# Performance work log

Measured on AMD Instinct MI355X. Metric: run time of the kernel, lower is better.

The kernel has to match this reference:

```python
import jax, jax.numpy as jnp
import numpy as np

B, N, DIM = 4, 2048, 1024
H, DH = 16, 64


def setup_inputs() -> dict:
    key = jax.random.key(0)
    k1, k2, k3 = jax.random.split(key, 3)
    x = jax.random.normal(k1, (B, N, DIM), dtype=jnp.float32)
    # nn.Linear weight layout: [out_features, in_features]; y = x @ W.T
    w_qkv = jax.random.normal(k2, (3 * H * DH, DIM), dtype=jnp.float32) * (DIM ** -0.5)
    w_out = jax.random.normal(k3, (DIM, H * DH), dtype=jnp.float32) * ((H * DH) ** -0.5)
    b_out = jnp.zeros((DIM,), dtype=jnp.float32)
    return {"x": x, "w_qkv": w_qkv, "w_out": w_out, "b_out": b_out}


def reference(x, w_qkv, w_out, b_out):
    scale = DH ** -0.5
    qkv = jnp.einsum('bnd,ed->bne', x, w_qkv)            # [B,N,3*H*DH]
    q, k, v = jnp.split(qkv, 3, axis=-1)
    def to_heads(t):
        return t.reshape(B, N, H, DH).transpose(0, 2, 1, 3)  # b h n d
    q, k, v = to_heads(q), to_heads(k), to_heads(v)
    scores = jnp.einsum('bhnd,bhmd->bhnm', q, k) * scale  # [B,H,N,N]
    att = jax.nn.softmax(scores, axis=-1)
    out = jnp.einsum('bhnm,bhmd->bhnd', att, v)
    out = out.transpose(0, 2, 1, 3).reshape(B, N, H * DH)  # b n (h d)
    return jnp.einsum('bne,de->bnd', out, w_out) + b_out
```

## Files before the change

### kernel.cpp

```cpp
#include <hip/hip_runtime.h>
#include <hip/hip_bf16.h>
#include <math.h>

#define B_   4
#define N_   2048
#define DIM_ 1024
#define H_   16
#define DH_  64
#define E3_  3072

typedef __attribute__((ext_vector_type(8))) short  s8v;
typedef __attribute__((ext_vector_type(4))) float  f4v;

__device__ __forceinline__ unsigned short f2bf_fast(float f) {
    return (unsigned short)((__builtin_bit_cast(unsigned int, f) + 0x8000u) >> 16);
}
__device__ __forceinline__ unsigned int pkbf(float a, float b) {
    unsigned int ua = __builtin_bit_cast(unsigned int, a) + 0x8000u;
    unsigned int ub = __builtin_bit_cast(unsigned int, b) + 0x8000u;
    return __builtin_amdgcn_perm(ub, ua, 0x07060302);
}

__device__ __forceinline__ void gload_lds16(const void* g, void* l) {
    __builtin_amdgcn_global_load_lds(
        (const __attribute__((address_space(1))) unsigned int*)(uintptr_t)g,
        (__attribute__((address_space(3))) unsigned int*)(uintptr_t)l,
        16, 0, 0);
}

__global__ __launch_bounds__(256) void cvt_bf16(
    const float* __restrict__ in, unsigned short* __restrict__ out, int n)
{
    const int i = (blockIdx.x * 256 + threadIdx.x) * 4;
    if (i < n) {
        float4 v = *(const float4*)(in + i);
        uint2 pk;
        pk.x = pkbf(v.x, v.y);
        pk.y = pkbf(v.z, v.w);
        *(uint2*)(out + i) = pk;
    }
}

template<int MODE>
__global__ __launch_bounds__(256) void gemm_mfma(
    const unsigned short* __restrict__ A,
    const unsigned short* __restrict__ Bw,
    const float* __restrict__ bias,
    unsigned short* __restrict__ Cb,
    unsigned short* __restrict__ Vt,
    float* __restrict__ Cf,
    int M, int Nc, int K)
{
    __shared__ unsigned short As[128 * 32];
    __shared__ unsigned short Bs[128 * 32];

    const int tid  = threadIdx.x;
    const int w    = tid >> 6;
    const int lane = tid & 63;
    const int quad = lane >> 4;
    const int l15  = lane & 15;
    const int wm   = w & 1, wn = w >> 1;
    const int m0   = blockIdx.y * 128, n0 = blockIdx.x * 128;

    const int srow = lane >> 2;
    const int sch  = (lane & 3) * 8;

    f4v acc[4][4];
    #pragma unroll
    for (int i = 0; i < 4; i++)
        #pragma unroll
        for (int j = 0; j < 4; j++) acc[i][j] = (f4v){0.f, 0.f, 0.f, 0.f};

    for (int k0 = 0; k0 < K; k0 += 32) {
        __syncthreads();
        #pragma unroll
        for (int i = 0; i < 2; i++) {
            const int rbase = w * 32 + i * 16;
            gload_lds16(A  + (size_t)(m0 + rbase + srow) * K + k0 + sch,
                        &As[rbase * 32]);
            gload_lds16(Bw + (size_t)(n0 + rbase + srow) * K + k0 + sch,
                        &Bs[rbase * 32]);
        }
        __syncthreads();

        s8v af[4], bf[4];
        #pragma unroll
        for (int i = 0; i < 4; i++) {
            af[i] = *(const s8v*)&As[(wm * 64 + i * 16 + l15) * 32 + quad * 8];
            bf[i] = *(const s8v*)&Bs[(wn * 64 + i * 16 + l15) * 32 + quad * 8];
        }
        #pragma unroll
        for (int ms = 0; ms < 4; ms++)
            #pragma unroll
            for (int ns = 0; ns < 4; ns++)
                acc[ms][ns] = __builtin_amdgcn_mfma_f32_16x16x32_bf16(
                    af[ms], bf[ns], acc[ms][ns], 0, 0, 0);
    }

    if (MODE == 0) {
        #pragma unroll
        for (int ns = 0; ns < 4; ns++) {
            const int colb = n0 + wn * 64 + ns * 16;
            if (colb < 2048) {
                const float mul = (colb < 1024) ? 0.18033688011112042f : 1.0f;
                #pragma unroll
                for (int ms = 0; ms < 4; ms++)
                    #pragma unroll
                    for (int r = 0; r < 4; r++) {
                        const int row = m0 + wm * 64 + ms * 16 + quad * 4 + r;
                        Cb[(size_t)row * Nc + colb + l15] = f2bf_fast(acc[ms][ns][r] * mul);
                    }
            } else {
                const int e = colb + l15 - 2048;
                const int h = e >> 6, d = e & 63;
                #pragma unroll
                for (int ms = 0; ms < 4; ms++) {
                    const int row = m0 + wm * 64 + ms * 16 + quad * 4;
                    const int b = row >> 11, n = row & 2047;
                    uint2 pk;
                    pk.x = pkbf(acc[ms][ns][0], acc[ms][ns][1]);
                    pk.y = pkbf(acc[ms][ns][2], acc[ms][ns][3]);
                    *(uint2*)&Vt[(((size_t)b * 16 + h) * 64 + d) * 2048 + n] = pk;
                }
            }
        }
    } else {
        #pragma unroll
        for (int ns = 0; ns < 4; ns++) {
            const float bz = bias[n0 + wn * 64 + ns * 16 + l15];
            #pragma unroll
            for (int ms = 0; ms < 4; ms++)
                #pragma unroll
                for (int r = 0; r < 4; r++) {
                    const int row = m0 + wm * 64 + ms * 16 + quad * 4 + r;
                    Cf[(size_t)row * Nc + n0 + wn * 64 + ns * 16 + l15] =
                        acc[ms][ns][r] + bz;
                }
        }
    }
}

__global__ __launch_bounds__(256, 2) void attn_mfma(
    const unsigned short* __restrict__ qkv,
    const unsigned short* __restrict__ vT,
    unsigned short* __restrict__ ao)
{
    __shared__ __align__(16) unsigned short Ks[2][64][72];
    __shared__ __align__(16) unsigned short Vs[2][64][72];
    __shared__ __align__(16) unsigned short Ps[256][72];

    const int tid  = threadIdx.x;
    const int w    = tid >> 6;
    const int lane = tid & 63;
    const int quad = lane >> 4;
    const int l15  = lane & 15;

    const int bh = blockIdx.y;
    const int b  = bh >> 4;
    const int h  = bh & 15;
    const int q0 = blockIdx.x * 256;

    const unsigned short* qp  = qkv + (size_t)b * N_ * E3_ + (size_t)h * DH_;
    const unsigned short* kp  = qp + 1024;
    const unsigned short* vtp = vT + (size_t)bh * 64 * 2048;

    const int srow0 = tid >> 3;
    const int srow1 = (tid + 256) >> 3;
    const int sc8   = (tid & 7) * 8;

    s8v bq[4][2];
    #pragma unroll
    for (int mt = 0; mt < 4; mt++) {
        const unsigned short* qrow =
            qp + (size_t)(q0 + w * 64 + mt * 16 + l15) * E3_;
        bq[mt][0] = *(const s8v*)(qrow + quad * 8);
        bq[mt][1] = *(const s8v*)(qrow + 32 + quad * 8);
    }

    s8v ones;
    #pragma unroll
    for (int i = 0; i < 8; i++) ones[i] = (short)0x3F80;

    f4v o_acc[4][4];
    #pragma unroll
    for (int mt = 0; mt < 4; mt++)
        #pragma unroll
        for (int nt = 0; nt < 4; nt++) o_acc[mt][nt] = (f4v){0.f, 0.f, 0.f, 0.f};
    f4v lacc[4];
    #pragma unroll
    for (int mt = 0; mt < 4; mt++) lacc[mt] = (f4v){0.f, 0.f, 0.f, 0.f};

    {
        s8v k0a = *(const s8v*)(kp + (size_t)srow0 * E3_ + sc8);
        s8v k1a = *(const s8v*)(kp + (size_t)srow1 * E3_ + sc8);
        s8v v0a = *(const s8v*)(vtp + (size_t)srow0 * 2048 + sc8);
        s8v v1a = *(const s8v*)(vtp + (size_t)srow1 * 2048 + sc8);
        *(s8v*)&Ks[0][srow0][sc8] = k0a;
        *(s8v*)&Ks[0][srow1][sc8] = k1a;
        *(s8v*)&Vs[0][srow0][sc8] = v0a;
        *(s8v*)&Vs[0][srow1][sc8] = v1a;
    }
    __syncthreads();

    for (int kt = 0; kt < N_ / 64; kt++) {
        const int cur = kt & 1;
        const bool pre = (kt + 1 < N_ / 64);

        s8v pk0, pk1, pv0, pv1;
        if (pre) {
            const int kn = (kt + 1) * 64;
            pk0 = *(const s8v*)(kp + (size_t)(kn + srow0) * E3_ + sc8);
            pk1 = *(const s8v*)(kp + (size_t)(kn + srow1) * E3_ + sc8);
            pv0 = *(const s8v*)(vtp + (size_t)srow0 * 2048 + kn + sc8);
            pv1 = *(const s8v*)(vtp + (size_t)srow1 * 2048 + kn + sc8);
        }

        #pragma unroll
        for (int nt = 0; nt < 4; nt++) {
            const s8v ak0 = *(const s8v*)&Ks[cur][nt * 16 + l15][quad * 8];
            const s8v ak1 = *(const s8v*)&Ks[cur][nt * 16 + l15][32 + quad * 8];
            f4v stv[4];
            #pragma unroll
            for (int mt = 0; mt < 4; mt++) {
                stv[mt] = (f4v){0.f, 0.f, 0.f, 0.f};
                stv[mt] = __builtin_amdgcn_mfma_f32_16x16x32_bf16(ak0, bq[mt][0], stv[mt], 0, 0, 0);
                stv[mt] = __builtin_amdgcn_mfma_f32_16x16x32_bf16(ak1, bq[mt][1], stv[mt], 0, 0, 0);
            }
            #pragma unroll
            for (int mt = 0; mt < 4; mt++) {
                uint2 pkd;
                pkd.x = pkbf(__builtin_amdgcn_exp2f(stv[mt][0]),
                             __builtin_amdgcn_exp2f(stv[mt][1]));
                pkd.y = pkbf(__builtin_amdgcn_exp2f(stv[mt][2]),
                             __builtin_amdgcn_exp2f(stv[mt][3]));
                *(uint2*)&Ps[w * 64 + mt * 16 + l15][nt * 16 + quad * 4] = pkd;
            }
        }

        #pragma unroll
        for (int ks = 0; ks < 2; ks++) {
            s8v ap[4];
            #pragma unroll
            for (int mt = 0; mt < 4; mt++) {
                ap[mt] = *(const s8v*)&Ps[w * 64 + mt * 16 + l15][ks * 32 + quad * 8];
                lacc[mt] = __builtin_amdgcn_mfma_f32_16x16x32_bf16(ap[mt], ones, lacc[mt], 0, 0, 0);
            }
            #pragma unroll
            for (int nt = 0; nt < 4; nt++) {
                const s8v bv = *(const s8v*)&Vs[cur][nt * 16 + l15][ks * 32 + quad * 8];
                #pragma unroll
                for (int mt = 0; mt < 4; mt++)
                    o_acc[mt][nt] = __builtin_amdgcn_mfma_f32_16x16x32_bf16(ap[mt], bv, o_acc[mt][nt], 0, 0, 0);
            }
        }

        if (pre) {
            const int nxt = cur ^ 1;
            *(s8v*)&Ks[nxt][srow0][sc8] = pk0;
            *(s8v*)&Ks[nxt][srow1][sc8] = pk1;
            *(s8v*)&Vs[nxt][srow0][sc8] = pv0;
            *(s8v*)&Vs[nxt][srow1][sc8] = pv1;
        }
        __syncthreads();
    }

    #pragma unroll
    for (int mt = 0; mt < 4; mt++) {
        float inv[4];
        #pragma unroll
        for (int r = 0; r < 4; r++) inv[r] = 1.f / lacc[mt][r];
        #pragma unroll
        for (int nt = 0; nt < 4; nt++)
            #pragma unroll
            for (int r = 0; r < 4; r++) {
                const int row = w * 64 + mt * 16 + quad * 4 + r;
                ao[((size_t)b * N_ + q0 + row) * (H_ * DH_) + h * DH_ + nt * 16 + l15] =
                    f2bf_fast(o_acc[mt][nt][r] * inv[r]);
            }
    }
}

extern "C" void kernel_launch(void* const* d_in, const int* in_sizes, int n_in,
                              void* d_out, int out_size, void* d_ws, size_t ws_size,
                              hipStream_t stream) {
    const float* x     = (const float*)d_in[0];
    const float* w_qkv = (const float*)d_in[1];
    const float* w_out = (const float*)d_in[2];
    const float* b_out = (const float*)d_in[3];
    float* out = (float*)d_out;

    char* ws = (char*)d_ws;
    unsigned short* x_bf    = (unsigned short*)(ws);
    unsigned short* wqkv_bf = (unsigned short*)(ws + (((size_t)16) << 20));
    unsigned short* wout_bf = (unsigned short*)(ws + (((size_t)22) << 20));
    unsigned short* qkv_bf  = (unsigned short*)(ws + (((size_t)24) << 20));
    unsigned short* vT      = (unsigned short*)(ws + (((size_t)72) << 20));
    unsigned short* ao_bf   = (unsigned short*)(ws + (((size_t)88) << 20));

    const int M = B_ * N_;

    cvt_bf16<<<(M * DIM_) / 1024, 256, 0, stream>>>(x, x_bf, M * DIM_);
    cvt_bf16<<<(E3_ * DIM_) / 1024, 256, 0, stream>>>(w_qkv, wqkv_bf, E3_ * DIM_);
    cvt_bf16<<<(DIM_ * DIM_) / 1024, 256, 0, stream>>>(w_out, wout_bf, DIM_ * DIM_);

    {
        dim3 grid(E3_ / 128, M / 128);
        gemm_mfma<0><<<grid, 256, 0, stream>>>(x_bf, wqkv_bf, nullptr,
                                               qkv_bf, vT, nullptr, M, E3_, DIM_);
    }
    {
        dim3 grid(N_ / 256, B_ * H_);
        attn_mfma<<<grid, 256, 0, stream>>>(qkv_bf, vT, ao_bf);
    }
    {
        dim3 grid(DIM_ / 128, M / 128);
        gemm_mfma<1><<<grid, 256, 0, stream>>>(ao_bf, wout_bf, b_out,
                                               nullptr, nullptr, out, M, DIM_, DIM_);
    }
    (void)in_sizes; (void)n_in; (void)out_size; (void)ws_size;
}
```

Baseline: 292.0 us.

## Rewrite attention core with 32x32 MFMA and register-resident P via permlane swap

Switches the attention kernel from 16x16x32 to 32x32x16 bf16 MFMA tiles. The exponentiated score tile is kept in registers: it is packed with v_cvt_pk_bf16_f32 and reshuffled into A-operand layout with v_permlane32_swap, so the P round trip through shared memory goes away. K/V shared tiles drop their padding and use an XOR swizzle to avoid bank conflicts, and s_setprio is placed around the MFMA bursts. The goal is to cut LDS traffic and instruction count in the inner loop, at the cost of relying on exact register-layout correctness for the permlane shuffle and a larger per-thread accumulator footprint.

```diff
diff --git a/kernel.cpp b/kernel.cpp
--- a/kernel.cpp
+++ b/kernel.cpp
@@ -9,8 +9,9 @@
 #define DH_  64
 #define E3_  3072
 
-typedef __attribute__((ext_vector_type(8))) short  s8v;
-typedef __attribute__((ext_vector_type(4))) float  f4v;
+typedef __attribute__((ext_vector_type(8)))  short s8v;
+typedef __attribute__((ext_vector_type(4)))  float f4v;
+typedef __attribute__((ext_vector_type(16))) float f16v;
 
 __device__ __forceinline__ unsigned short f2bf_fast(float f) {
     return (unsigned short)((__builtin_bit_cast(unsigned int, f) + 0x8000u) >> 16);
@@ -19,6 +20,15 @@
     unsigned int ua = __builtin_bit_cast(unsigned int, a) + 0x8000u;
     unsigned int ub = __builtin_bit_cast(unsigned int, b) + 0x8000u;
     return __builtin_amdgcn_perm(ub, ua, 0x07060302);
+}
+__device__ __forceinline__ unsigned int cvtpk(float a, float b) {
+    unsigned int r;
+    asm("v_cvt_pk_bf16_f32 %0, %1, %2" : "=v"(r) : "v"(a), "v"(b));
+    return r;
+}
+__device__ __forceinline__ uint2 pl32(unsigned int a, unsigned int b) {
+    asm volatile("v_permlane32_swap_b32 %0, %1" : "+v"(a), "+v"(b));
+    return make_uint2(a, b);
 }
 
 __device__ __forceinline__ void gload_lds16(const void* g, void* l) {
@@ -145,15 +155,15 @@
     const unsigned short* __restrict__ vT,
     unsigned short* __restrict__ ao)
 {
-    __shared__ __align__(16) unsigned short Ks[2][64][72];
-    __shared__ __align__(16) unsigned short Vs[2][64][72];
-    __shared__ __align__(16) unsigned short Ps[256][72];
+    __shared__ __align__(16) unsigned short Ks[2][64][64];
+    __shared__ __align__(16) unsigned short Vs[2][64][64];
 
     const int tid  = threadIdx.x;
     const int w    = tid >> 6;
     const int lane = tid & 63;
-    const int quad = lane >> 4;
-    const int l15  = lane & 15;
+    const int l31  = lane & 31;
+    const int hi5  = lane >> 5;
+    const int h8   = hi5 * 8;
 
     const int bh = blockIdx.y;
     const int b  = bh >> 4;
@@ -165,40 +175,41 @@
     const unsigned short* vtp = vT + (size_t)bh * 64 * 2048;
 
     const int srow0 = tid >> 3;
-    const int srow1 = (tid + 256) >> 3;
-    const int sc8   = (tid & 7) * 8;
-
-    s8v bq[4][2];
+    const int srow1 = srow0 + 32;
+    const int sc    = tid & 7;
+    const int sw0   = (sc ^ (srow0 & 7)) * 8;
+    const int sw1   = (sc ^ (srow1 & 7)) * 8;
+
+    s8v bq[2][4];
     #pragma unroll
-    for (int mt = 0; mt < 4; mt++) {
+    for (int sub = 0; sub < 2; sub++) {
         const unsigned short* qrow =
-            qp + (size_t)(q0 + w * 64 + mt * 16 + l15) * E3_;
-        bq[mt][0] = *(const s8v*)(qrow + quad * 8);
-        bq[mt][1] = *(const s8v*)(qrow + 32 + quad * 8);
+            qp + (size_t)(q0 + w * 64 + sub * 32 + l31) * E3_;
+        #pragma unroll
+        for (int ks = 0; ks < 4; ks++)
+            bq[sub][ks] = *(const s8v*)(qrow + ks * 16 + h8);
     }
 
     s8v ones;
     #pragma unroll
     for (int i = 0; i < 8; i++) ones[i] = (short)0x3F80;
 
-    f4v o_acc[4][4];
-    #pragma unroll
-    for (int mt = 0; mt < 4; mt++)
-        #pragma unroll
-        for (int nt = 0; nt < 4; nt++) o_acc[mt][nt] = (f4v){0.f, 0.f, 0.f, 0.f};
-    f4v lacc[4];
-    #pragma unroll
-    for (int mt = 0; mt < 4; mt++) lacc[mt] = (f4v){0.f, 0.f, 0.f, 0.f};
+    const f16v fzero = {0.f,0.f,0.f,0.f,0.f,0.f,0.f,0.f,
+                        0.f,0.f,0.f,0.f,0.f,0.f,0.f,0.f};
+    f16v o[2][2];
+    o[0][0] = fzero; o[0][1] = fzero; o[1][0] = fzero; o[1][1] = fzero;
+    f16v lc[2];
+    lc[0] = fzero; lc[1] = fzero;
 
     {
-        s8v k0a = *(const s8v*)(kp + (size_t)srow0 * E3_ + sc8);
-        s8v k1a = *(const s8v*)(kp + (size_t)srow1 * E3_ + sc8);
-        s8v v0a = *(const s8v*)(vtp + (size_t)srow0 * 2048 + sc8);
-        s8v v1a = *(const s8v*)(vtp + (size_t)srow1 * 2048 + sc8);
-        *(s8v*)&Ks[0][srow0][sc8] = k0a;
-        *(s8v*)&Ks[0][srow1][sc8] = k1a;
-        *(s8v*)&Vs[0][srow0][sc8] = v0a;
-        *(s8v*)&Vs[0][srow1][sc8] = v1a;
+        s8v k0 = *(const s8v*)(kp  + (size_t)srow0 * E3_  + sc * 8);
+        s8v k1 = *(const s8v*)(kp  + (size_t)srow1 * E3_  + sc * 8);
+        s8v v0 = *(const s8v*)(vtp + (size_t)srow0 * 2048 + sc * 8);
+        s8v v1 = *(const s8v*)(vtp + (size_t)srow1 * 2048 + sc * 8);
+        *(s8v*)&Ks[0][srow0][sw0] = k0;
+        *(s8v*)&Ks[0][srow1][sw1] = k1;
+        *(s8v*)&Vs[0][srow0][sw0] = v0;
+        *(s8v*)&Vs[0][srow1][sw1] = v1;
     }
     __syncthreads();
 
@@ -209,73 +220,90 @@
         s8v pk0, pk1, pv0, pv1;
         if (pre) {
             const int kn = (kt + 1) * 64;
-            pk0 = *(const s8v*)(kp + (size_t)(kn + srow0) * E3_ + sc8);
-            pk1 = *(const s8v*)(kp + (size_t)(kn + srow1) * E3_ + sc8);
-            pv0 = *(const s8v*)(vtp + (size_t)srow0 * 2048 + kn + sc8);
-            pv1 = *(const s8v*)(vtp + (size_t)srow1 * 2048 + kn + sc8);
-        }
-
-        #pragma unroll
-        for (int nt = 0; nt < 4; nt++) {
-            const s8v ak0 = *(const s8v*)&Ks[cur][nt * 16 + l15][quad * 8];
-            const s8v ak1 = *(const s8v*)&Ks[cur][nt * 16 + l15][32 + quad * 8];
-            f4v stv[4];
-            #pragma unroll
-            for (int mt = 0; mt < 4; mt++) {
-                stv[mt] = (f4v){0.f, 0.f, 0.f, 0.f};
-                stv[mt] = __builtin_amdgcn_mfma_f32_16x16x32_bf16(ak0, bq[mt][0], stv[mt], 0, 0, 0);
-                stv[mt] = __builtin_amdgcn_mfma_f32_16x16x32_bf16(ak1, bq[mt][1], stv[mt], 0, 0, 0);
+            pk0 = *(const s8v*)(kp  + (size_t)(kn + srow0) * E3_ + sc * 8);
+            pk1 = *(const s8v*)(kp  + (size_t)(kn + srow1) * E3_ + sc * 8);
+            pv0 = *(const s8v*)(vtp + (size_t)srow0 * 2048 + kn + sc * 8);
+            pv1 = *(const s8v*)(vtp + (size_t)srow1 * 2048 + kn + sc * 8);
+        }
+
+        #pragma unroll
+        for (int ksub = 0; ksub < 2; ksub++) {
+            const int krow = ksub * 32 + l31;
+            const int ksw  = (krow & 7) * 8;
+            s8v ak[4];
+            #pragma unroll
+            for (int ks = 0; ks < 4; ks++)
+                ak[ks] = *(const s8v*)&Ks[cur][krow][(ks * 16 + h8) ^ ksw];
+
+            s8v pa[2][2];
+            #pragma unroll
+            for (int sub = 0; sub < 2; sub++) {
+                f16v st = fzero;
+                __builtin_amdgcn_s_setprio(1);
+                st = __builtin_amdgcn_mfma_f32_32x32x16_bf16(ak[0], bq[sub][0], st, 0, 0, 0);
+                st = __builtin_amdgcn_mfma_f32_32x32x16_bf16(ak[1], bq[sub][1], st, 0, 0, 0);
+                st = __builtin_amdgcn_mfma_f32_32x32x16_bf16(ak[2], bq[sub][2], st, 0, 0, 0);
+                st = __builtin_amdgcn_mfma_f32_32x32x16_bf16(ak[3], bq[sub][3], st, 0, 0, 0);
+                __builtin_amdgcn_s_setprio(0);
+
+                float pe[16];
+                #pragma unroll
+                for (int i = 0; i < 16; i++)
+                    pe[i] = __builtin_amdgcn_exp2f(st[i]);
+
+                union { s8v v; unsigned int u[4]; } f0, f1;
+                uint2 r;
+                r = pl32(cvtpk(pe[0],  pe[1]),  cvtpk(pe[4],  pe[5]));
+                f0.u[0] = r.x; f0.u[2] = r.y;
+                r = pl32(cvtpk(pe[2],  pe[3]),  cvtpk(pe[6],  pe[7]));
+                f0.u[1] = r.x; f0.u[3] = r.y;
+                r = pl32(cvtpk(pe[8],  pe[9]),  cvtpk(pe[12], pe[13]));
+                f1.u[0] = r.x; f1.u[2] = r.y;
+                r = pl32(cvtpk(pe[10], pe[11]), cvtpk(pe[14], pe[15]));
+                f1.u[1] = r.x; f1.u[3] = r.y;
+                pa[sub][0] = f0.v;
+                pa[sub][1] = f1.v;
             }
-            #pragma unroll
-            for (int mt = 0; mt < 4; mt++) {
-                uint2 pkd;
-                pkd.x = pkbf(__builtin_amdgcn_exp2f(stv[mt][0]),
-                             __builtin_amdgcn_exp2f(stv[mt][1]));
-                pkd.y = pkbf(__builtin_amdgcn_exp2f(stv[mt][2]),
-                             __builtin_amdgcn_exp2f(stv[mt][3]));
-                *(uint2*)&Ps[w * 64 + mt * 16 + l15][nt * 16 + quad * 4] = pkd;
-            }
-        }
-
-        #pragma unroll
-        for (int ks = 0; ks < 2; ks++) {
-            s8v ap[4];
-            #pragma unroll
-            for (int mt = 0; mt < 4; mt++) {
-                ap[mt] = *(const s8v*)&Ps[w * 64 + mt * 16 + l15][ks * 32 + quad * 8];
-                lacc[mt] = __builtin_amdgcn_mfma_f32_16x16x32_bf16(ap[mt], ones, lacc[mt], 0, 0, 0);
-            }
-            #pragma unroll
-            for (int nt = 0; nt < 4; nt++) {
-                const s8v bv = *(const s8v*)&Vs[cur][nt * 16 + l15][ks * 32 + quad * 8];
-                #pragma unroll
-                for (int mt = 0; mt < 4; mt++)
-                    o_acc[mt][nt] = __builtin_amdgcn_mfma_f32_16x16x32_bf16(ap[mt], bv, o_acc[mt][nt], 0, 0, 0);
+
+            #pragma unroll
+            for (int j = 0; j < 2; j++) {
+                const int kbase = (ksub * 2 + j) * 16 + h8;
+                const int vsw   = (l31 & 7) * 8;
+                s8v bv0 = *(const s8v*)&Vs[cur][l31     ][kbase ^ vsw];
+                s8v bv1 = *(const s8v*)&Vs[cur][32 + l31][kbase ^ vsw];
+                __builtin_amdgcn_s_setprio(1);
+                o[0][0] = __builtin_amdgcn_mfma_f32_32x32x16_bf16(pa[0][j], bv0, o[0][0], 0, 0, 0);
+                o[1][0] = __builtin_amdgcn_mfma_f32_32x32x16_bf16(pa[1][j], bv0, o[1][0], 0, 0, 0);
+                o[0][1] = __builtin_amdgcn_mfma_f32_32x32x16_bf16(pa[0][j], bv1, o[0][1], 0, 0, 0);
+                o[1][1] = __builtin_amdgcn_mfma_f32_32x32x16_bf16(pa[1][j], bv1, o[1][1], 0, 0, 0);
+                lc[0]   = __builtin_amdgcn_mfma_f32_32x32x16_bf16(pa[0][j], ones, lc[0], 0, 0, 0);
+                lc[1]   = __builtin_amdgcn_mfma_f32_32x32x16_bf16(pa[1][j], ones, lc[1], 0, 0, 0);
+                __builtin_amdgcn_s_setprio(0);
             }
         }
 
         if (pre) {
             const int nxt = cur ^ 1;
-            *(s8v*)&Ks[nxt][srow0][sc8] = pk0;
-            *(s8v*)&Ks[nxt][srow1][sc8] = pk1;
-            *(s8v*)&Vs[nxt][srow0][sc8] = pv0;
-            *(s8v*)&Vs[nxt][srow1][sc8] = pv1;
+            *(s8v*)&Ks[nxt][srow0][sw0] = pk0;
+            *(s8v*)&Ks[nxt][srow1][sw1] = pk1;
+            *(s8v*)&Vs[nxt][srow0][sw0] = pv0;
+            *(s8v*)&Vs[nxt][srow1][sw1] = pv1;
         }
         __syncthreads();
     }
 
     #pragma unroll
-    for (int mt = 0; mt < 4; mt++) {
-        float inv[4];
-        #pragma unroll
-        for (int r = 0; r < 4; r++) inv[r] = 1.f / lacc[mt][r];
-        #pragma unroll
-        for (int nt = 0; nt < 4; nt++)
-            #pragma unroll
-            for (int r = 0; r < 4; r++) {
-                const int row = w * 64 + mt * 16 + quad * 4 + r;
-                ao[((size_t)b * N_ + q0 + row) * (H_ * DH_) + h * DH_ + nt * 16 + l15] =
-                    f2bf_fast(o_acc[mt][nt][r] * inv[r]);
+    for (int sub = 0; sub < 2; sub++) {
+        float inv[16];
+        #pragma unroll
+        for (int r = 0; r < 16; r++) inv[r] = 1.f / lc[sub][r];
+        #pragma unroll
+        for (int dt = 0; dt < 2; dt++)
+            #pragma unroll
+            for (int r = 0; r < 16; r++) {
+                const int qrow = q0 + w * 64 + sub * 32 + (r & 3) + 8 * (r >> 2) + 4 * hi5;
+                ao[((size_t)b * N_ + qrow) * (H_ * DH_) + h * DH_ + dt * 32 + l31] =
+                    f2bf_fast(o[sub][dt][r] * inv[r]);
             }
     }
 }
```

After: 285.3 us. -2.3%, faster.
